# Kernel optimization log

Hardware: AMD Instinct MI355X
Metric: run time of the kernel (lower is better)

Reference implementation:

```python
import jax, jax.numpy as jnp
import numpy as np

HEADS = 8
POINTS = 4
EPS = 1e-5


def _layernorm(x, w, b):
    m = jnp.mean(x, axis=-1, keepdims=True)
    v = jnp.var(x, axis=-1, keepdims=True)
    return (x - m) / jnp.sqrt(v + EPS) * w + b


def _msdeform_attn(x, ref, value, H, W, Wv, bv, Woff, boff, Wa, ba, Wout, bout):
    # x: (N, Lq, C) queries; value: (N, H*W, C); ref: (N, Lq, 1, 2) in [0,1]
    N, Lq, C = x.shape
    hd = C // HEADS
    # value projection, split heads -> (N, heads, HW, hd)
    v = (value @ Wv + bv).reshape(N, H * W, HEADS, hd).transpose(0, 2, 1, 3)
    # per-query learned offsets and attention weights
    off = (x @ Woff + boff).reshape(N, Lq, HEADS, POINTS, 2)
    attw = jax.nn.softmax((x @ Wa + ba).reshape(N, Lq, HEADS, POINTS), axis=-1)
    offset_normalizer = jnp.array([W, H], dtype=x.dtype)
    # sampling locations in normalized [0,1] coords: (N, Lq, heads, points, 2)
    loc = ref[:, :, None, :, :] + off / offset_normalizer
    # grid_sample bilinear, align_corners=False, zeros padding: pixel = loc*size - 0.5
    gx = loc[..., 0] * W - 0.5
    gy = loc[..., 1] * H - 0.5
    x0 = jnp.floor(gx)
    y0 = jnp.floor(gy)
    wx = gx - x0
    wy = gy - y0
    x0i = x0.astype(jnp.int32)
    y0i = y0.astype(jnp.int32)

    def gather(xi, yi):  # (N,Lq,heads,points) int -> (N,heads,Lq,points,hd), zero outside
        valid = ((xi >= 0) & (xi < W) & (yi >= 0) & (yi < H))
        idx = (jnp.clip(yi, 0, H - 1) * W + jnp.clip(xi, 0, W - 1)).transpose(0, 2, 1, 3)
        g = jnp.take_along_axis(v, idx.reshape(N, HEADS, Lq * POINTS)[..., None], axis=2)
        return g.reshape(N, HEADS, Lq, POINTS, hd) * valid.transpose(0, 2, 1, 3)[..., None].astype(v.dtype)

    def cw(w_):  # corner weight to (N,heads,Lq,points,1)
        return w_.transpose(0, 2, 1, 3)[..., None]

    samp = (gather(x0i, y0i) * cw((1 - wx) * (1 - wy))
            + gather(x0i + 1, y0i) * cw(wx * (1 - wy))
            + gather(x0i, y0i + 1) * cw((1 - wx) * wy)
            + gather(x0i + 1, y0i + 1) * cw(wx * wy))
    out = jnp.einsum('nhlpd,nlhp->nlhd', samp, attw).reshape(N, Lq, C)
    return out @ Wout + bout


def setup_inputs() -> dict:
    key = jax.random.key(0)
    ks = jax.random.split(key, 12)
    N, Lq, C, H, W = 4, 6400, 256, 80, 80
    hid = 4 * C
    hp2 = HEADS * POINTS * 2
    hp = HEADS * POINTS

    def w(k, shape, s=0.02):
        return jax.random.normal(k, shape, dtype=jnp.float32) * s

    return {
        'x': jax.random.normal(ks[0], (N, Lq, C), dtype=jnp.float32),
        'ref': jax.random.uniform(ks[1], (N, Lq, 1, 2), dtype=jnp.float32),
        'value': jax.random.normal(ks[2], (N, Lq, C), dtype=jnp.float32),
        'H': H, 'W': W,
        'ln1_w': jnp.ones((C,), jnp.float32), 'ln1_b': jnp.zeros((C,), jnp.float32),
        'ln2_w': jnp.ones((C,), jnp.float32), 'ln2_b': jnp.zeros((C,), jnp.float32),
        'Wv': w(ks[3], (C, C)), 'bv': jnp.zeros((C,), jnp.float32),
        'Woff': w(ks[4], (C, hp2), 0.01), 'boff': w(ks[5], (hp2,), 0.5),
        'Wa': w(ks[6], (C, hp)), 'ba': jnp.zeros((hp,), jnp.float32),
        'Wout': w(ks[7], (C, C)), 'bout': jnp.zeros((C,), jnp.float32),
        'W1': w(ks[8], (C, hid)), 'b1': jnp.zeros((hid,), jnp.float32),
        'W2': w(ks[9], (hid, C)), 'b2': jnp.zeros((C,), jnp.float32),
    }


def reference(x, ref, value, H, W, ln1_w, ln1_b, ln2_w, ln2_b, Wv, bv, Woff, boff, Wa, ba, Wout, bout, W1, b1, W2, b2):
    # x = x + attn(norm1(x), ref, value); LayerScale/DropPath are identity (init_values=None, drop_path=0)
    a = _msdeform_attn(_layernorm(x, ln1_w, ln1_b), ref, value, H, W, Wv, bv, Woff, boff, Wa, ba, Wout, bout)
    x = x + a
    # x = x + mlp(norm2(x))
    h = _layernorm(x, ln2_w, ln2_b)
    h = jax.nn.gelu(h @ W1 + b1, approximate=False)
    return x + (h @ W2 + b2)
```

## Files before the change

### kernel.cpp

```cpp
#include <hip/hip_runtime.h>

#define NB    4
#define LQ    6400
#define CC    256
#define HH    80
#define WW    80
#define HWSZ  (HH*WW)
#define RTOT  (NB*LQ)
#define HID   1024

typedef __attribute__((ext_vector_type(8))) short bf16x8;
typedef __attribute__((ext_vector_type(4))) float f32x4;

__device__ __forceinline__ float bf2f(unsigned short u) {
    unsigned int i = ((unsigned int)u) << 16;
    float f; __builtin_memcpy(&f, &i, 4); return f;
}
__device__ __forceinline__ unsigned short f2bf(float f) {
    unsigned int i; __builtin_memcpy(&i, &f, 4);
    unsigned int r = i + 0x7fffu + ((i >> 16) & 1u);
    return (unsigned short)(r >> 16);
}

__global__ void cvt_k(const float* __restrict__ in, unsigned short* __restrict__ out, int n4) {
    int i = blockIdx.x * 256 + threadIdx.x;
    if (i < n4) {
        float4 u = ((const float4*)in)[i];
        ushort4 o;
        o.x = f2bf(u.x); o.y = f2bf(u.y); o.z = f2bf(u.z); o.w = f2bf(u.w);
        ((ushort4*)out)[i] = o;
    }
}

__global__ void transpose_cvt_k(const float* __restrict__ B,
                                unsigned short* __restrict__ Bt, int K, int N) {
    int idx = blockIdx.x * 256 + threadIdx.x;
    if (idx < K * N) {
        int n = idx / K;
        int k = idx - n * K;
        Bt[idx] = f2bf(B[k * N + n]);
    }
}

__global__ void swizzle_k(const float* __restrict__ src, unsigned short* __restrict__ dst,
                          int K, int N) {
    int g = blockIdx.x * 256 + threadIdx.x;
    if (g >= (K / 8) * N) return;
    int n  = g % N;
    int kq = g / N;
    int kbase = (kq >> 2) * 32 + (kq & 3) * 8;
    unsigned short* d = dst + (size_t)g * 8;
    #pragma unroll
    for (int j = 0; j < 8; ++j)
        d[j] = f2bf(src[(size_t)(kbase + j) * N + n]);
}

__global__ void bias_cat_k(const float* __restrict__ boff, const float* __restrict__ ba,
                           float* __restrict__ out) {
    int i = threadIdx.x;
    if (i < 64) out[i] = boff[i];
    else if (i < 96) out[i] = ba[i - 64];
}

__global__ void ln_k(const float* __restrict__ x,
                     const float* __restrict__ w,
                     const float* __restrict__ b,
                     unsigned short* __restrict__ y) {
    int row  = blockIdx.x * 4 + (threadIdx.x >> 6);
    int lane = threadIdx.x & 63;
    const float* xr = x + (size_t)row * CC + lane * 4;
    float4 u = *(const float4*)xr;
    float s  = u.x + u.y + u.z + u.w;
    float s2 = u.x*u.x + u.y*u.y + u.z*u.z + u.w*u.w;
    #pragma unroll
    for (int m = 1; m < 64; m <<= 1) {
        s  += __shfl_xor(s,  m);
        s2 += __shfl_xor(s2, m);
    }
    float mean = s * (1.0f / CC);
    float var  = s2 * (1.0f / CC) - mean * mean;
    float rstd = rsqrtf(fmaxf(var, 0.0f) + 1e-5f);
    float4 uw = *(const float4*)(w + lane * 4);
    float4 ub = *(const float4*)(b + lane * 4);
    ushort4 o;
    o.x = f2bf((u.x - mean) * rstd * uw.x + ub.x);
    o.y = f2bf((u.y - mean) * rstd * uw.y + ub.y);
    o.z = f2bf((u.z - mean) * rstd * uw.z + ub.z);
    o.w = f2bf((u.w - mean) * rstd * uw.w + ub.w);
    *(ushort4*)(y + (size_t)row * CC + lane * 4) = o;
}

template<int EPI, bool OF32>
__global__ __launch_bounds__(256) void gemm_t(const unsigned short* __restrict__ A,
                                              const unsigned short* __restrict__ Bt,
                                              const float* __restrict__ bias,
                                              const float* __restrict__ res,
                                              void* __restrict__ Cout_,
                                              int M, int Nv, int K) {
    __shared__ unsigned short Als[64 * 32];
    __shared__ unsigned short Bls[128 * 32];
    int lane = threadIdx.x & 63;
    int wave = threadIdx.x >> 6;
    int quad = lane >> 4;
    int l16  = lane & 15;
    int m0 = blockIdx.x * 64;
    int n0 = blockIdx.y * 128;
    int wm = (wave & 1) * 32;
    int wn = (wave >> 1) * 64;

    f32x4 acc[2][4];
    #pragma unroll
    for (int i = 0; i < 2; ++i)
        #pragma unroll
        for (int j = 0; j < 4; ++j)
            acc[i][j] = (f32x4){0.f, 0.f, 0.f, 0.f};

    int srow = lane >> 2;
    int scol = (lane & 3) * 8;
    const unsigned short* Ag = A  + (size_t)(m0 + wave * 16 + srow) * K + scol;
    const unsigned short* Bg = Bt + (size_t)(n0 + wave * 32 + srow) * K + scol;
    unsigned short* Alp = &Als[wave * 512];
    unsigned short* Blp = &Bls[wave * 1024];

    for (int k0 = 0; k0 < K; k0 += 32) {
        __syncthreads();
        __builtin_amdgcn_global_load_lds(
            (const __attribute__((address_space(1))) void*)(Ag + k0),
            (__attribute__((address_space(3))) void*)Alp, 16, 0, 0);
        #pragma unroll
        for (int t = 0; t < 2; ++t) {
            __builtin_amdgcn_global_load_lds(
                (const __attribute__((address_space(1))) void*)(Bg + (size_t)t * 16 * K + k0),
                (__attribute__((address_space(3))) void*)(Blp + t * 512), 16, 0, 0);
        }
        __builtin_amdgcn_s_waitcnt(0);
        __syncthreads();

        bf16x8 af[2], bfr[4];
        #pragma unroll
        for (int i = 0; i < 2; ++i)
            af[i] = *(const bf16x8*)&Als[(wm + i * 16 + l16) * 32 + quad * 8];
        #pragma unroll
        for (int j = 0; j < 4; ++j)
            bfr[j] = *(const bf16x8*)&Bls[(wn + j * 16 + l16) * 32 + quad * 8];
        #pragma unroll
        for (int i = 0; i < 2; ++i)
            #pragma unroll
            for (int j = 0; j < 4; ++j)
                acc[i][j] = __builtin_amdgcn_mfma_f32_16x16x32_bf16(af[i], bfr[j], acc[i][j], 0, 0, 0);
    }

    #pragma unroll
    for (int j = 0; j < 4; ++j) {
        int cbase = n0 + wn + j * 16;
        if (cbase >= Nv) continue;
        int col = cbase + l16;
        float bv = bias[col];
        #pragma unroll
        for (int i = 0; i < 2; ++i) {
            #pragma unroll
            for (int r = 0; r < 4; ++r) {
                int row = m0 + wm + i * 16 + quad * 4 + r;
                float val = acc[i][j][r] + bv;
                if (EPI == 2) val += res[(size_t)row * Nv + col];
                if (OF32) ((float*)Cout_)[(size_t)row * Nv + col] = val;
                else      ((unsigned short*)Cout_)[(size_t)row * Nv + col] = f2bf(val);
            }
        }
    }
}

__global__ __launch_bounds__(256) void sample_k(
        const unsigned short* __restrict__ v,
        const float* __restrict__ ref,
        const unsigned short* __restrict__ oa,
        unsigned short* __restrict__ samp) {
    __shared__ int4   sidx[256];
    __shared__ float4 sw[256];

    int t = threadIdx.x;
    int row0 = blockIdx.x * 8;
    int n = blockIdx.x / (LQ / 8);

    {
        int q = t >> 5;
        int h = (t >> 2) & 7;
        int p = t & 3;
        int row = row0 + q;
        float refx = ref[row * 2 + 0];
        float refy = ref[row * 2 + 1];
        const unsigned short* oar = oa + (size_t)row * 96;
        float ox = bf2f(oar[(h * 4 + p) * 2 + 0]);
        float oy = bf2f(oar[(h * 4 + p) * 2 + 1]);
        float l  = bf2f(oar[64 + h * 4 + p]);
        float m = fmaxf(l, __shfl_xor(l, 1));
        m = fmaxf(m, __shfl_xor(m, 2));
        float e = __expf(l - m);
        float s = e + __shfl_xor(e, 1);
        s = s + __shfl_xor(s, 2);
        float wp = e / s;

        float gx = (refx + ox * (1.0f / WW)) * WW - 0.5f;
        float gy = (refy + oy * (1.0f / HH)) * HH - 0.5f;
        float fx = floorf(gx), fy = floorf(gy);
        float wx = gx - fx, wy = gy - fy;
        int x0 = (int)fx, y0 = (int)fy;
        int x1 = x0 + 1, y1 = y0 + 1;
        bool vx0 = (unsigned)x0 < WW, vx1 = (unsigned)x1 < WW;
        bool vy0 = (unsigned)y0 < HH, vy1 = (unsigned)y1 < HH;
        float w00 = (vx0 && vy0) ? wp * (1.f - wx) * (1.f - wy) : 0.f;
        float w10 = (vx1 && vy0) ? wp * wx * (1.f - wy)         : 0.f;
        float w01 = (vx0 && vy1) ? wp * (1.f - wx) * wy         : 0.f;
        float w11 = (vx1 && vy1) ? wp * wx * wy                 : 0.f;
        int cx0 = min(max(x0, 0), WW - 1), cx1 = min(max(x1, 0), WW - 1);
        int cy0 = min(max(y0, 0), HH - 1), cy1 = min(max(y1, 0), HH - 1);
        sidx[t] = (int4){cy0 * WW + cx0, cy0 * WW + cx1, cy1 * WW + cx0, cy1 * WW + cx1};
        sw[t]   = (float4){w00, w10, w01, w11};
    }
    __syncthreads();

    int q  = t >> 5;
    int sub = t & 31;
    int h  = sub >> 2;
    int cg = sub & 3;
    int row = row0 + q;
    const unsigned short* base = v + (size_t)n * HWSZ * CC + h * 32 + cg * 8;

    float acc[8];
    #pragma unroll
    for (int j = 0; j < 8; ++j) acc[j] = 0.f;

    #pragma unroll
    for (int p = 0; p < 4; ++p) {
        int e = ((q * 8 + h) * 4) + p;
        int4   I = sidx[e];
        float4 Wt = sw[e];
        const int* Ip = (const int*)&I;
        const float* Wp = (const float*)&Wt;
        #pragma unroll
        for (int c = 0; c < 4; ++c) {
            bf16x8 u = *(const bf16x8*)(base + (size_t)Ip[c] * CC);
            float wgt = Wp[c];
            #pragma unroll
            for (int j = 0; j < 8; ++j)
                acc[j] += wgt * bf2f((unsigned short)u[j]);
        }
    }

    bf16x8 o;
    #pragma unroll
    for (int j = 0; j < 8; ++j) o[j] = (short)f2bf(acc[j]);
    *(bf16x8*)(samp + (size_t)row * CC + h * 32 + cg * 8) = o;
}

__global__ __launch_bounds__(512) void mlp_k(
        const float* __restrict__ x2,
        const float* __restrict__ lw,
        const float* __restrict__ lb,
        const unsigned short* __restrict__ w1s,
        const float* __restrict__ b1,
        const unsigned short* __restrict__ w2s,
        const float* __restrict__ b2,
        float* __restrict__ out) {
    __shared__ char lds_raw[66560];
    unsigned short* hblob = (unsigned short*)lds_raw;
    unsigned short* h1b0  = (unsigned short*)(lds_raw + 33280);
    unsigned short* h1b1  = (unsigned short*)(lds_raw + 49920);
    float* trans = (float*)lds_raw;

    int t = threadIdx.x;
    int lane = t & 63, wave = t >> 6;
    int quad = lane >> 4, l16 = lane & 15;
    int row0 = blockIdx.x * 64;

    {
        int r = t >> 3, sub = t & 7;
        const float* xr = x2 + (size_t)(row0 + r) * CC;
        float4 xv[4][2];
        float s = 0.f, s2 = 0.f;
        #pragma unroll
        for (int jj = 0; jj < 4; ++jj) {
            #pragma unroll
            for (int u = 0; u < 2; ++u) {
                float4 v = *(const float4*)(xr + sub * 8 + jj * 64 + u * 4);
                xv[jj][u] = v;
                s  += v.x + v.y + v.z + v.w;
                s2 += v.x*v.x + v.y*v.y + v.z*v.z + v.w*v.w;
            }
        }
        #pragma unroll
        for (int m = 1; m < 8; m <<= 1) {
            s  += __shfl_xor(s,  m);
            s2 += __shfl_xor(s2, m);
        }
        float mean = s * (1.0f / CC);
        float var  = s2 * (1.0f / CC) - mean * mean;
        float rstd = rsqrtf(fmaxf(var, 0.0f) + 1e-5f);
        #pragma unroll
        for (int jj = 0; jj < 4; ++jj) {
            int c0 = sub * 8 + jj * 64;
            float4 w0 = *(const float4*)(lw + c0);
            float4 w1 = *(const float4*)(lw + c0 + 4);
            float4 bb0 = *(const float4*)(lb + c0);
            float4 bb1 = *(const float4*)(lb + c0 + 4);
            bf16x8 o;
            o[0] = (short)f2bf((xv[jj][0].x - mean) * rstd * w0.x + bb0.x);
            o[1] = (short)f2bf((xv[jj][0].y - mean) * rstd * w0.y + bb0.y);
            o[2] = (short)f2bf((xv[jj][0].z - mean) * rstd * w0.z + bb0.z);
            o[3] = (short)f2bf((xv[jj][0].w - mean) * rstd * w0.w + bb0.w);
            o[4] = (short)f2bf((xv[jj][1].x - mean) * rstd * w1.x + bb1.x);
            o[5] = (short)f2bf((xv[jj][1].y - mean) * rstd * w1.y + bb1.y);
            o[6] = (short)f2bf((xv[jj][1].z - mean) * rstd * w1.z + bb1.z);
            o[7] = (short)f2bf((xv[jj][1].w - mean) * rstd * w1.w + bb1.w);
            int kq = sub + jj * 8;
            *(bf16x8*)((char*)hblob + kq * 1040 + r * 16) = o;
        }
    }
    __syncthreads();

    f32x4 acc2[2][4];
    #pragma unroll
    for (int a = 0; a < 2; ++a)
        #pragma unroll
        for (int b = 0; b < 4; ++b)
            acc2[a][b] = (f32x4){0.f, 0.f, 0.f, 0.f};

    auto s1 = [&](int hc, unsigned short* dst) {
        f32x4 a[4];
        #pragma unroll
        for (int qt = 0; qt < 4; ++qt) a[qt] = (f32x4){0.f, 0.f, 0.f, 0.f};
        #pragma unroll
        for (int kb = 0; kb < 8; ++kb) {
            bf16x8 a1 = *(const bf16x8*)(w1s + ((size_t)(kb * 4 + quad) * 1024 + hc * 128 + wave * 16 + l16) * 8);
            #pragma unroll
            for (int qt = 0; qt < 4; ++qt) {
                bf16x8 bf = *(const bf16x8*)((char*)hblob + (kb * 4 + quad) * 1040 + (qt * 16 + l16) * 16);
                a[qt] = __builtin_amdgcn_mfma_f32_16x16x32_bf16(a1, bf, a[qt], 0, 0, 0);
            }
        }
        int hl = wave * 16 + quad * 4;
        float4 bb = *(const float4*)(b1 + hc * 128 + hl);
        const float* bp = (const float*)&bb;
        #pragma unroll
        for (int qt = 0; qt < 4; ++qt) {
            unsigned long long pk = 0;
            #pragma unroll
            for (int r = 0; r < 4; ++r) {
                float val = a[qt][r] + bp[r];
                val = 0.5f * val * (1.0f + erff(val * 0.70710678118654752f));
                pk |= ((unsigned long long)f2bf(val)) << (16 * r);
            }
            *(unsigned long long*)((char*)dst + (hl >> 3) * 1040 + (qt * 16 + l16) * 16 + (hl & 7) * 2) = pk;
        }
    };

    auto s2 = [&](int hc, const unsigned short* src) {
        #pragma unroll
        for (int k2 = 0; k2 < 4; ++k2) {
            bf16x8 a2[2], bf[4];
            #pragma unroll
            for (int ct = 0; ct < 2; ++ct)
                a2[ct] = *(const bf16x8*)(w2s + ((size_t)((hc * 4 + k2) * 4 + quad) * 256 + wave * 32 + ct * 16 + l16) * 8);
            #pragma unroll
            for (int qt = 0; qt < 4; ++qt)
                bf[qt] = *(const bf16x8*)((const char*)src + (k2 * 4 + quad) * 1040 + (qt * 16 + l16) * 16);
            #pragma unroll
            for (int ct = 0; ct < 2; ++ct)
                #pragma unroll
                for (int qt = 0; qt < 4; ++qt)
                    acc2[ct][qt] = __builtin_amdgcn_mfma_f32_16x16x32_bf16(a2[ct], bf[qt], acc2[ct][qt], 0, 0, 0);
        }
    };

    s1(0, h1b0);
    for (int hc = 0; hc < 8; ++hc) {
        __syncthreads();
        const unsigned short* cur = (hc & 1) ? h1b1 : h1b0;
        unsigned short*       nxt = (hc & 1) ? h1b0 : h1b1;
        s2(hc, cur);
        if (hc < 7) s1(hc + 1, nxt);
    }
    __syncthreads();

    #pragma unroll
    for (int qt = 0; qt < 4; ++qt) {
        int qrow = qt * 16 + l16;
        #pragma unroll
        for (int ct = 0; ct < 2; ++ct) {
            int c4 = wave * 8 + ct * 4 + quad;
            *(f32x4*)(trans + qrow * 260 + c4 * 4) = acc2[ct][qt];
        }
    }
    __syncthreads();
    {
        int rr = t >> 3;
        int c4b = t & 7;
        int row = row0 + rr;
        #pragma unroll
        for (int i = 0; i < 8; ++i) {
            int c4 = i * 8 + c4b;
            f32x4 v = *(const f32x4*)(trans + rr * 260 + c4 * 4);
            int c = c4 * 4;
            float4 xv = *(const float4*)(x2 + (size_t)row * CC + c);
            float4 bb = *(const float4*)(b2 + c);
            float4 o;
            o.x = v[0] + xv.x + bb.x;
            o.y = v[1] + xv.y + bb.y;
            o.z = v[2] + xv.z + bb.z;
            o.w = v[3] + xv.w + bb.w;
            *(float4*)(out + (size_t)row * CC + c) = o;
        }
    }
}

extern "C" void kernel_launch(void* const* d_in, const int* in_sizes, int n_in,
                              void* d_out, int out_size, void* d_ws, size_t ws_size,
                              hipStream_t stream) {
    const float* x     = (const float*)d_in[0];
    const float* ref   = (const float*)d_in[1];
    const float* value = (const float*)d_in[2];
    const float* ln1w  = (const float*)d_in[5];
    const float* ln1b  = (const float*)d_in[6];
    const float* ln2w  = (const float*)d_in[7];
    const float* ln2b  = (const float*)d_in[8];
    const float* Wv    = (const float*)d_in[9];
    const float* bv    = (const float*)d_in[10];
    const float* Woff  = (const float*)d_in[11];
    const float* boff  = (const float*)d_in[12];
    const float* Wa    = (const float*)d_in[13];
    const float* ba    = (const float*)d_in[14];
    const float* Wout  = (const float*)d_in[15];
    const float* bout  = (const float*)d_in[16];
    const float* W1    = (const float*)d_in[17];
    const float* b1    = (const float*)d_in[18];
    const float* W2    = (const float*)d_in[19];
    const float* b2    = (const float*)d_in[20];

    char* ws = (char*)d_ws;
    unsigned short* wt_v  = (unsigned short*)(ws + 0);
    unsigned short* wt_o  = (unsigned short*)(ws + 131072);
    unsigned short* w1s_b = (unsigned short*)(ws + 262144);
    unsigned short* w2s_b = (unsigned short*)(ws + 786432);
    unsigned short* wt_oa = (unsigned short*)(ws + 1310720);
    float*          b_oa  = (float*)         (ws + 1376256);
    float*          x2_f  = (float*)         (ws + 1376768);
    unsigned short* val_b = (unsigned short*)(ws + 40698368);
    unsigned short* smp_b = (unsigned short*)(ws + 40698368);
    unsigned short* xn_b  = (unsigned short*)(ws + 53805568);
    unsigned short* v_b   = (unsigned short*)(ws + 66912768);
    unsigned short* oa_b  = (unsigned short*)(ws + 80019968);

    transpose_cvt_k<<<(256*256 + 255) / 256, 256, 0, stream>>>(Wv,   wt_v,           256, 256);
    transpose_cvt_k<<<(256*256 + 255) / 256, 256, 0, stream>>>(Wout, wt_o,           256, 256);
    transpose_cvt_k<<<(256*64  + 255) / 256, 256, 0, stream>>>(Woff, wt_oa,          256, 64);
    transpose_cvt_k<<<(256*32  + 255) / 256, 256, 0, stream>>>(Wa,   wt_oa + 64*256, 256, 32);
    swizzle_k<<<128, 256, 0, stream>>>(W1, w1s_b, 256, 1024);
    swizzle_k<<<128, 256, 0, stream>>>(W2, w2s_b, 1024, 256);
    bias_cat_k<<<1, 128, 0, stream>>>(boff, ba, b_oa);

    cvt_k<<<(RTOT*CC/4 + 255) / 256, 256, 0, stream>>>(value, val_b, RTOT*CC/4);
    ln_k<<<RTOT / 4, 256, 0, stream>>>(x, ln1w, ln1b, xn_b);

    dim3 blk(256);
    gemm_t<0, false><<<dim3(RTOT/64, 2), blk, 0, stream>>>(val_b, wt_v,  bv,   nullptr, v_b,  RTOT, 256,  256);
    gemm_t<0, false><<<dim3(RTOT/64, 1), blk, 0, stream>>>(xn_b,  wt_oa, b_oa, nullptr, oa_b, RTOT, 96,   256);
    sample_k<<<RTOT / 8, 256, 0, stream>>>(v_b, ref, oa_b, smp_b);
    gemm_t<2, true ><<<dim3(RTOT/64, 2), blk, 0, stream>>>(smp_b, wt_o,  bout, x,       x2_f, RTOT, 256,  256);
    mlp_k<<<RTOT / 64, 512, 0, stream>>>(x2_f, ln2w, ln2b, w1s_b, b1, w2s_b, b2, (float*)d_out);
}
```

Before: 248.3 us.

## Fuse LN1 with offset/attn GEMM and sampling with output projection

Merges the seven weight-prep launches into a single prep kernel. It fuses LayerNorm1 with the offset/attention-logit projection into one MFMA kernel, and fuses bilinear sampling with the Wout projection and residual add. The sampled tile stays in LDS, so neither the normalized activations nor the sampled features make a round trip through global memory. Sample indices are packed to short4 to save LDS. The cost is larger LDS per block, fewer resident blocks, and idle waves in the 96-column GEMM.

```diff
diff --git a/kernel.cpp b/kernel.cpp
--- a/kernel.cpp
+++ b/kernel.cpp
@@ -32,62 +32,109 @@
     }
 }
 
-__global__ void transpose_cvt_k(const float* __restrict__ B,
-                                unsigned short* __restrict__ Bt, int K, int N) {
+__global__ void prep_k(const float* __restrict__ Wv,   const float* __restrict__ Wout,
+                       const float* __restrict__ W1,   const float* __restrict__ W2,
+                       const float* __restrict__ Woff, const float* __restrict__ Wa,
+                       const float* __restrict__ boff, const float* __restrict__ ba,
+                       unsigned short* __restrict__ wtv,  unsigned short* __restrict__ woutS,
+                       unsigned short* __restrict__ w1s,  unsigned short* __restrict__ w2s,
+                       unsigned short* __restrict__ woas, float* __restrict__ b_oa) {
     int idx = blockIdx.x * 256 + threadIdx.x;
-    if (idx < K * N) {
-        int n = idx / K;
-        int k = idx - n * K;
-        Bt[idx] = f2bf(B[k * N + n]);
-    }
-}
-
-__global__ void swizzle_k(const float* __restrict__ src, unsigned short* __restrict__ dst,
-                          int K, int N) {
-    int g = blockIdx.x * 256 + threadIdx.x;
-    if (g >= (K / 8) * N) return;
-    int n  = g % N;
-    int kq = g / N;
-    int kbase = (kq >> 2) * 32 + (kq & 3) * 8;
-    unsigned short* d = dst + (size_t)g * 8;
-    #pragma unroll
-    for (int j = 0; j < 8; ++j)
-        d[j] = f2bf(src[(size_t)(kbase + j) * N + n]);
-}
-
-__global__ void bias_cat_k(const float* __restrict__ boff, const float* __restrict__ ba,
-                           float* __restrict__ out) {
-    int i = threadIdx.x;
-    if (i < 64) out[i] = boff[i];
-    else if (i < 96) out[i] = ba[i - 64];
-}
-
-__global__ void ln_k(const float* __restrict__ x,
-                     const float* __restrict__ w,
-                     const float* __restrict__ b,
-                     unsigned short* __restrict__ y) {
-    int row  = blockIdx.x * 4 + (threadIdx.x >> 6);
-    int lane = threadIdx.x & 63;
-    const float* xr = x + (size_t)row * CC + lane * 4;
-    float4 u = *(const float4*)xr;
-    float s  = u.x + u.y + u.z + u.w;
-    float s2 = u.x*u.x + u.y*u.y + u.z*u.z + u.w*u.w;
-    #pragma unroll
-    for (int m = 1; m < 64; m <<= 1) {
+    if (idx < 65536) {
+        int n = idx >> 8, k = idx & 255;
+        wtv[idx] = f2bf(Wv[(size_t)k * 256 + n]);
+        return;
+    }
+    idx -= 65536;
+    if (idx < 32768) {
+        int n = idx & 1023, kq = idx >> 10;
+        int kb = (kq >> 2) * 32 + (kq & 3) * 8;
+        unsigned short* d = w1s + (size_t)idx * 8;
+        #pragma unroll
+        for (int j = 0; j < 8; ++j) d[j] = f2bf(W1[(size_t)(kb + j) * 1024 + n]);
+        return;
+    }
+    idx -= 32768;
+    if (idx < 32768) {
+        int n = idx & 255, kq = idx >> 8;
+        int kb = (kq >> 2) * 32 + (kq & 3) * 8;
+        unsigned short* d = w2s + (size_t)idx * 8;
+        #pragma unroll
+        for (int j = 0; j < 8; ++j) d[j] = f2bf(W2[(size_t)(kb + j) * 256 + n]);
+        return;
+    }
+    idx -= 32768;
+    if (idx < 8192) {
+        int n = idx & 255, kq = idx >> 8;
+        int kb = (kq >> 2) * 32 + (kq & 3) * 8;
+        unsigned short* d = woutS + (size_t)idx * 8;
+        #pragma unroll
+        for (int j = 0; j < 8; ++j) d[j] = f2bf(Wout[(size_t)(kb + j) * 256 + n]);
+        return;
+    }
+    idx -= 8192;
+    if (idx < 4096) {
+        int n = idx & 127, kq = idx >> 7;
+        int kb = (kq >> 2) * 32 + (kq & 3) * 8;
+        unsigned short* d = woas + (size_t)idx * 8;
+        #pragma unroll
+        for (int j = 0; j < 8; ++j) {
+            float v = 0.f;
+            if (n < 64)      v = Woff[(size_t)(kb + j) * 64 + n];
+            else if (n < 96) v = Wa[(size_t)(kb + j) * 32 + (n - 64)];
+            d[j] = f2bf(v);
+        }
+        return;
+    }
+    idx -= 4096;
+    if (idx < 96) b_oa[idx] = idx < 64 ? boff[idx] : ba[idx - 64];
+}
+
+__device__ __forceinline__ void ln_stage(const float* __restrict__ xbase,
+                                         const float* __restrict__ lw,
+                                         const float* __restrict__ lb,
+                                         unsigned short* hblob, int t) {
+    int r = t >> 3, sub = t & 7;
+    const float* xr = xbase + (size_t)r * CC;
+    float4 xv[4][2];
+    float s = 0.f, s2 = 0.f;
+    #pragma unroll
+    for (int jj = 0; jj < 4; ++jj) {
+        #pragma unroll
+        for (int u = 0; u < 2; ++u) {
+            float4 v = *(const float4*)(xr + sub * 8 + jj * 64 + u * 4);
+            xv[jj][u] = v;
+            s  += v.x + v.y + v.z + v.w;
+            s2 += v.x*v.x + v.y*v.y + v.z*v.z + v.w*v.w;
+        }
+    }
+    #pragma unroll
+    for (int m = 1; m < 8; m <<= 1) {
         s  += __shfl_xor(s,  m);
         s2 += __shfl_xor(s2, m);
     }
     float mean = s * (1.0f / CC);
     float var  = s2 * (1.0f / CC) - mean * mean;
     float rstd = rsqrtf(fmaxf(var, 0.0f) + 1e-5f);
-    float4 uw = *(const float4*)(w + lane * 4);
-    float4 ub = *(const float4*)(b + lane * 4);
-    ushort4 o;
-    o.x = f2bf((u.x - mean) * rstd * uw.x + ub.x);
-    o.y = f2bf((u.y - mean) * rstd * uw.y + ub.y);
-    o.z = f2bf((u.z - mean) * rstd * uw.z + ub.z);
-    o.w = f2bf((u.w - mean) * rstd * uw.w + ub.w);
-    *(ushort4*)(y + (size_t)row * CC + lane * 4) = o;
+    #pragma unroll
+    for (int jj = 0; jj < 4; ++jj) {
+        int c0 = sub * 8 + jj * 64;
+        float4 w0 = *(const float4*)(lw + c0);
+        float4 w1 = *(const float4*)(lw + c0 + 4);
+        float4 bb0 = *(const float4*)(lb + c0);
+        float4 bb1 = *(const float4*)(lb + c0 + 4);
+        bf16x8 o;
+        o[0] = (short)f2bf((xv[jj][0].x - mean) * rstd * w0.x + bb0.x);
+        o[1] = (short)f2bf((xv[jj][0].y - mean) * rstd * w0.y + bb0.y);
+        o[2] = (short)f2bf((xv[jj][0].z - mean) * rstd * w0.z + bb0.z);
+        o[3] = (short)f2bf((xv[jj][0].w - mean) * rstd * w0.w + bb0.w);
+        o[4] = (short)f2bf((xv[jj][1].x - mean) * rstd * w1.x + bb1.x);
+        o[5] = (short)f2bf((xv[jj][1].y - mean) * rstd * w1.y + bb1.y);
+        o[6] = (short)f2bf((xv[jj][1].z - mean) * rstd * w1.z + bb1.z);
+        o[7] = (short)f2bf((xv[jj][1].w - mean) * rstd * w1.w + bb1.w);
+        int kq = sub + jj * 8;
+        *(bf16x8*)((char*)hblob + kq * 1040 + r * 16) = o;
+    }
 }
 
 template<int EPI, bool OF32>
@@ -170,87 +217,191 @@
     }
 }
 
-__global__ __launch_bounds__(256) void sample_k(
+__global__ __launch_bounds__(512) void lnoa_k(
+        const float* __restrict__ x, const float* __restrict__ lw, const float* __restrict__ lb,
+        const unsigned short* __restrict__ woas, const float* __restrict__ b_oa,
+        unsigned short* __restrict__ oa) {
+    __shared__ char lds_raw[33280];
+    unsigned short* hblob = (unsigned short*)lds_raw;
+    int t = threadIdx.x;
+    int lane = t & 63, wave = t >> 6;
+    int quad = lane >> 4, l16 = lane & 15;
+    int row0 = blockIdx.x * 64;
+
+    ln_stage(x + (size_t)row0 * CC, lw, lb, hblob, t);
+    __syncthreads();
+
+    if (wave < 6) {
+        f32x4 acc[4];
+        #pragma unroll
+        for (int qt = 0; qt < 4; ++qt) acc[qt] = (f32x4){0.f, 0.f, 0.f, 0.f};
+        #pragma unroll
+        for (int kb = 0; kb < 8; ++kb) {
+            bf16x8 a1 = *(const bf16x8*)(woas + ((size_t)(kb * 4 + quad) * 128 + wave * 16 + l16) * 8);
+            #pragma unroll
+            for (int qt = 0; qt < 4; ++qt) {
+                bf16x8 bf = *(const bf16x8*)((char*)hblob + (kb * 4 + quad) * 1040 + (qt * 16 + l16) * 16);
+                acc[qt] = __builtin_amdgcn_mfma_f32_16x16x32_bf16(a1, bf, acc[qt], 0, 0, 0);
+            }
+        }
+        int n0 = wave * 16 + quad * 4;
+        float4 bb = *(const float4*)(b_oa + n0);
+        const float* bp = (const float*)&bb;
+        #pragma unroll
+        for (int qt = 0; qt < 4; ++qt) {
+            unsigned long long pk = 0;
+            #pragma unroll
+            for (int r = 0; r < 4; ++r)
+                pk |= ((unsigned long long)f2bf(acc[qt][r] + bp[r])) << (16 * r);
+            *(unsigned long long*)(oa + (size_t)(row0 + qt * 16 + l16) * 96 + n0) = pk;
+        }
+    }
+}
+
+__global__ __launch_bounds__(512) void samwout_k(
         const unsigned short* __restrict__ v,
         const float* __restrict__ ref,
         const unsigned short* __restrict__ oa,
-        unsigned short* __restrict__ samp) {
-    __shared__ int4   sidx[256];
-    __shared__ float4 sw[256];
+        const unsigned short* __restrict__ woutS,
+        const float* __restrict__ bout,
+        const float* __restrict__ x,
+        float* __restrict__ x2) {
+    __shared__ char lds_raw[57856];
+    unsigned short* hblob = (unsigned short*)lds_raw;
+    short4* sidx = (short4*)(lds_raw + 33280);
+    float4* sw   = (float4*)(lds_raw + 41472);
+    float* trans = (float*)lds_raw;
 
     int t = threadIdx.x;
-    int row0 = blockIdx.x * 8;
-    int n = blockIdx.x / (LQ / 8);
-
-    {
-        int q = t >> 5;
-        int h = (t >> 2) & 7;
-        int p = t & 3;
-        int row = row0 + q;
-        float refx = ref[row * 2 + 0];
-        float refy = ref[row * 2 + 1];
-        const unsigned short* oar = oa + (size_t)row * 96;
-        float ox = bf2f(oar[(h * 4 + p) * 2 + 0]);
-        float oy = bf2f(oar[(h * 4 + p) * 2 + 1]);
-        float l  = bf2f(oar[64 + h * 4 + p]);
-        float m = fmaxf(l, __shfl_xor(l, 1));
-        m = fmaxf(m, __shfl_xor(m, 2));
-        float e = __expf(l - m);
-        float s = e + __shfl_xor(e, 1);
-        s = s + __shfl_xor(s, 2);
-        float wp = e / s;
-
-        float gx = (refx + ox * (1.0f / WW)) * WW - 0.5f;
-        float gy = (refy + oy * (1.0f / HH)) * HH - 0.5f;
-        float fx = floorf(gx), fy = floorf(gy);
-        float wx = gx - fx, wy = gy - fy;
-        int x0 = (int)fx, y0 = (int)fy;
-        int x1 = x0 + 1, y1 = y0 + 1;
-        bool vx0 = (unsigned)x0 < WW, vx1 = (unsigned)x1 < WW;
-        bool vy0 = (unsigned)y0 < HH, vy1 = (unsigned)y1 < HH;
-        float w00 = (vx0 && vy0) ? wp * (1.f - wx) * (1.f - wy) : 0.f;
-        float w10 = (vx1 && vy0) ? wp * wx * (1.f - wy)         : 0.f;
-        float w01 = (vx0 && vy1) ? wp * (1.f - wx) * wy         : 0.f;
-        float w11 = (vx1 && vy1) ? wp * wx * wy                 : 0.f;
-        int cx0 = min(max(x0, 0), WW - 1), cx1 = min(max(x1, 0), WW - 1);
-        int cy0 = min(max(y0, 0), HH - 1), cy1 = min(max(y1, 0), HH - 1);
-        sidx[t] = (int4){cy0 * WW + cx0, cy0 * WW + cx1, cy1 * WW + cx0, cy1 * WW + cx1};
-        sw[t]   = (float4){w00, w10, w01, w11};
-    }
-    __syncthreads();
-
-    int q  = t >> 5;
-    int sub = t & 31;
-    int h  = sub >> 2;
-    int cg = sub & 3;
-    int row = row0 + q;
-    const unsigned short* base = v + (size_t)n * HWSZ * CC + h * 32 + cg * 8;
-
-    float acc[8];
-    #pragma unroll
-    for (int j = 0; j < 8; ++j) acc[j] = 0.f;
-
-    #pragma unroll
-    for (int p = 0; p < 4; ++p) {
-        int e = ((q * 8 + h) * 4) + p;
-        int4   I = sidx[e];
-        float4 Wt = sw[e];
-        const int* Ip = (const int*)&I;
-        const float* Wp = (const float*)&Wt;
-        #pragma unroll
-        for (int c = 0; c < 4; ++c) {
-            bf16x8 u = *(const bf16x8*)(base + (size_t)Ip[c] * CC);
-            float wgt = Wp[c];
-            #pragma unroll
-            for (int j = 0; j < 8; ++j)
-                acc[j] += wgt * bf2f((unsigned short)u[j]);
-        }
-    }
-
-    bf16x8 o;
-    #pragma unroll
-    for (int j = 0; j < 8; ++j) o[j] = (short)f2bf(acc[j]);
-    *(bf16x8*)(samp + (size_t)row * CC + h * 32 + cg * 8) = o;
+    int lane = t & 63, wave = t >> 6;
+    int quad = lane >> 4, l16 = lane & 15;
+    int row0 = blockIdx.x * 64;
+    int nb = blockIdx.x / (LQ / 64);
+
+    for (int half = 0; half < 2; ++half) {
+        int rbase = half * 32;
+        #pragma unroll
+        for (int s = 0; s < 2; ++s) {
+            int e = t + s * 512;
+            int q = e >> 5, sub = e & 31, h = sub >> 2, p = sub & 3;
+            int row = row0 + rbase + q;
+            float refx = ref[row * 2 + 0];
+            float refy = ref[row * 2 + 1];
+            const unsigned short* oar = oa + (size_t)row * 96;
+            float ox = bf2f(oar[(h * 4 + p) * 2 + 0]);
+            float oy = bf2f(oar[(h * 4 + p) * 2 + 1]);
+            float l  = bf2f(oar[64 + h * 4 + p]);
+            float m = fmaxf(l, __shfl_xor(l, 1));
+            m = fmaxf(m, __shfl_xor(m, 2));
+            float ee = __expf(l - m);
+            float ss = ee + __shfl_xor(ee, 1);
+            ss = ss + __shfl_xor(ss, 2);
+            float wp = ee / ss;
+
+            float gx = (refx + ox * (1.0f / WW)) * WW - 0.5f;
+            float gy = (refy + oy * (1.0f / HH)) * HH - 0.5f;
+            float fx = floorf(gx), fy = floorf(gy);
+            float wx = gx - fx, wy = gy - fy;
+            int x0 = (int)fx, y0 = (int)fy;
+            int x1 = x0 + 1, y1 = y0 + 1;
+            bool vx0 = (unsigned)x0 < WW, vx1 = (unsigned)x1 < WW;
+            bool vy0 = (unsigned)y0 < HH, vy1 = (unsigned)y1 < HH;
+            float w00 = (vx0 && vy0) ? wp * (1.f - wx) * (1.f - wy) : 0.f;
+            float w10 = (vx1 && vy0) ? wp * wx * (1.f - wy)         : 0.f;
+            float w01 = (vx0 && vy1) ? wp * (1.f - wx) * wy         : 0.f;
+            float w11 = (vx1 && vy1) ? wp * wx * wy                 : 0.f;
+            int cx0 = min(max(x0, 0), WW - 1), cx1 = min(max(x1, 0), WW - 1);
+            int cy0 = min(max(y0, 0), HH - 1), cy1 = min(max(y1, 0), HH - 1);
+            sidx[e] = (short4){(short)(cy0 * WW + cx0), (short)(cy0 * WW + cx1),
+                               (short)(cy1 * WW + cx0), (short)(cy1 * WW + cx1)};
+            sw[e]   = (float4){w00, w10, w01, w11};
+        }
+        __syncthreads();
+        #pragma unroll
+        for (int s = 0; s < 2; ++s) {
+            int c = t + s * 512;
+            int q = c >> 5, sub = c & 31, h = sub >> 2, cg = sub & 3;
+            const unsigned short* base = v + (size_t)nb * HWSZ * CC + h * 32 + cg * 8;
+            float acc[8];
+            #pragma unroll
+            for (int j = 0; j < 8; ++j) acc[j] = 0.f;
+            #pragma unroll
+            for (int p = 0; p < 4; ++p) {
+                int e = q * 32 + h * 4 + p;
+                short4 I = sidx[e];
+                float4 Wt = sw[e];
+                const short* Ip = (const short*)&I;
+                const float* Wp = (const float*)&Wt;
+                #pragma unroll
+                for (int cn = 0; cn < 4; ++cn) {
+                    bf16x8 u = *(const bf16x8*)(base + (size_t)(unsigned short)Ip[cn] * CC);
+                    float wgt = Wp[cn];
+                    #pragma unroll
+                    for (int j = 0; j < 8; ++j)
+                        acc[j] += wgt * bf2f((unsigned short)u[j]);
+                }
+            }
+            bf16x8 o;
+            #pragma unroll
+            for (int j = 0; j < 8; ++j) o[j] = (short)f2bf(acc[j]);
+            *(bf16x8*)((char*)hblob + sub * 1040 + (rbase + q) * 16) = o;
+        }
+        __syncthreads();
+    }
+
+    f32x4 acc2[2][4];
+    #pragma unroll
+    for (int a = 0; a < 2; ++a)
+        #pragma unroll
+        for (int b = 0; b < 4; ++b)
+            acc2[a][b] = (f32x4){0.f, 0.f, 0.f, 0.f};
+    #pragma unroll
+    for (int kb = 0; kb < 8; ++kb) {
+        bf16x8 a2[2], bf[4];
+        #pragma unroll
+        for (int ct = 0; ct < 2; ++ct)
+            a2[ct] = *(const bf16x8*)(woutS + ((size_t)(kb * 4 + quad) * 256 + wave * 32 + ct * 16 + l16) * 8);
+        #pragma unroll
+        for (int qt = 0; qt < 4; ++qt)
+            bf[qt] = *(const bf16x8*)((char*)hblob + (kb * 4 + quad) * 1040 + (qt * 16 + l16) * 16);
+        #pragma unroll
+        for (int ct = 0; ct < 2; ++ct)
+            #pragma unroll
+            for (int qt = 0; qt < 4; ++qt)
+                acc2[ct][qt] = __builtin_amdgcn_mfma_f32_16x16x32_bf16(a2[ct], bf[qt], acc2[ct][qt], 0, 0, 0);
+    }
+
+    for (int p = 0; p < 2; ++p) {
+        __syncthreads();
+        #pragma unroll
+        for (int qi = 0; qi < 2; ++qi) {
+            int qt = p * 2 + qi;
+            int qlocal = qt * 16 + l16 - p * 32;
+            #pragma unroll
+            for (int ct = 0; ct < 2; ++ct) {
+                int c4 = wave * 8 + ct * 4 + quad;
+                *(f32x4*)(trans + qlocal * 260 + c4 * 4) = acc2[ct][qt];
+            }
+        }
+        __syncthreads();
+        int rr = t >> 4;
+        int c4b = t & 15;
+        int row = row0 + p * 32 + rr;
+        #pragma unroll
+        for (int i = 0; i < 4; ++i) {
+            int c4 = i * 16 + c4b;
+            f32x4 vv = *(const f32x4*)(trans + rr * 260 + c4 * 4);
+            int c = c4 * 4;
+            float4 xv = *(const float4*)(x + (size_t)row * CC + c);
+            float4 bb = *(const float4*)(bout + c);
+            float4 o;
+            o.x = vv[0] + xv.x + bb.x;
+            o.y = vv[1] + xv.y + bb.y;
+            o.z = vv[2] + xv.z + bb.z;
+            o.w = vv[3] + xv.w + bb.w;
+            *(float4*)(x2 + (size_t)row * CC + c) = o;
+        }
+    }
 }
 
 __global__ __launch_bounds__(512) void mlp_k(
@@ -273,49 +424,7 @@
     int quad = lane >> 4, l16 = lane & 15;
     int row0 = blockIdx.x * 64;
 
-    {
-        int r = t >> 3, sub = t & 7;
-        const float* xr = x2 + (size_t)(row0 + r) * CC;
-        float4 xv[4][2];
-        float s = 0.f, s2 = 0.f;
-        #pragma unroll
-        for (int jj = 0; jj < 4; ++jj) {
-            #pragma unroll
-            for (int u = 0; u < 2; ++u) {
-                float4 v = *(const float4*)(xr + sub * 8 + jj * 64 + u * 4);
-                xv[jj][u] = v;
-                s  += v.x + v.y + v.z + v.w;
-                s2 += v.x*v.x + v.y*v.y + v.z*v.z + v.w*v.w;
-            }
-        }
-        #pragma unroll
-        for (int m = 1; m < 8; m <<= 1) {
-            s  += __shfl_xor(s,  m);
-            s2 += __shfl_xor(s2, m);
-        }
-        float mean = s * (1.0f / CC);
-        float var  = s2 * (1.0f / CC) - mean * mean;
-        float rstd = rsqrtf(fmaxf(var, 0.0f) + 1e-5f);
-        #pragma unroll
-        for (int jj = 0; jj < 4; ++jj) {
-            int c0 = sub * 8 + jj * 64;
-            float4 w0 = *(const float4*)(lw + c0);
-            float4 w1 = *(const float4*)(lw + c0 + 4);
-            float4 bb0 = *(const float4*)(lb + c0);
-            float4 bb1 = *(const float4*)(lb + c0 + 4);
-            bf16x8 o;
-            o[0] = (short)f2bf((xv[jj][0].x - mean) * rstd * w0.x + bb0.x);
-            o[1] = (short)f2bf((xv[jj][0].y - mean) * rstd * w0.y + bb0.y);
-            o[2] = (short)f2bf((xv[jj][0].z - mean) * rstd * w0.z + bb0.z);
-            o[3] = (short)f2bf((xv[jj][0].w - mean) * rstd * w0.w + bb0.w);
-            o[4] = (short)f2bf((xv[jj][1].x - mean) * rstd * w1.x + bb1.x);
-            o[5] = (short)f2bf((xv[jj][1].y - mean) * rstd * w1.y + bb1.y);
-            o[6] = (short)f2bf((xv[jj][1].z - mean) * rstd * w1.z + bb1.z);
-            o[7] = (short)f2bf((xv[jj][1].w - mean) * rstd * w1.w + bb1.w);
-            int kq = sub + jj * 8;
-            *(bf16x8*)((char*)hblob + kq * 1040 + r * 16) = o;
-        }
-    }
+    ln_stage(x2 + (size_t)row0 * CC, lw, lb, hblob, t);
     __syncthreads();
 
     f32x4 acc2[2][4];
@@ -437,34 +546,22 @@
     const float* b2    = (const float*)d_in[20];
 
     char* ws = (char*)d_ws;
-    unsigned short* wt_v  = (unsigned short*)(ws + 0);
-    unsigned short* wt_o  = (unsigned short*)(ws + 131072);
-    unsigned short* w1s_b = (unsigned short*)(ws + 262144);
-    unsigned short* w2s_b = (unsigned short*)(ws + 786432);
-    unsigned short* wt_oa = (unsigned short*)(ws + 1310720);
-    float*          b_oa  = (float*)         (ws + 1376256);
-    float*          x2_f  = (float*)         (ws + 1376768);
-    unsigned short* val_b = (unsigned short*)(ws + 40698368);
-    unsigned short* smp_b = (unsigned short*)(ws + 40698368);
-    unsigned short* xn_b  = (unsigned short*)(ws + 53805568);
-    unsigned short* v_b   = (unsigned short*)(ws + 66912768);
-    unsigned short* oa_b  = (unsigned short*)(ws + 80019968);
-
-    transpose_cvt_k<<<(256*256 + 255) / 256, 256, 0, stream>>>(Wv,   wt_v,           256, 256);
-    transpose_cvt_k<<<(256*256 + 255) / 256, 256, 0, stream>>>(Wout, wt_o,           256, 256);
-    transpose_cvt_k<<<(256*64  + 255) / 256, 256, 0, stream>>>(Woff, wt_oa,          256, 64);
-    transpose_cvt_k<<<(256*32  + 255) / 256, 256, 0, stream>>>(Wa,   wt_oa + 64*256, 256, 32);
-    swizzle_k<<<128, 256, 0, stream>>>(W1, w1s_b, 256, 1024);
-    swizzle_k<<<128, 256, 0, stream>>>(W2, w2s_b, 1024, 256);
-    bias_cat_k<<<1, 128, 0, stream>>>(boff, ba, b_oa);
-
+    unsigned short* wtv_b  = (unsigned short*)(ws + 0);
+    unsigned short* wouts_b= (unsigned short*)(ws + 131072);
+    unsigned short* w1s_b  = (unsigned short*)(ws + 262144);
+    unsigned short* w2s_b  = (unsigned short*)(ws + 786432);
+    unsigned short* woas_b = (unsigned short*)(ws + 1310720);
+    float*          b_oa   = (float*)         (ws + 1376256);
+    float*          x2_f   = (float*)         (ws + 1376768);
+    unsigned short* val_b  = (unsigned short*)(ws + 27591168);
+    unsigned short* v_b    = (unsigned short*)(ws + 40698368);
+    unsigned short* oa_b   = (unsigned short*)(ws + 53805568);
+
+    prep_k<<<561, 256, 0, stream>>>(Wv, Wout, W1, W2, Woff, Wa, boff, ba,
+                                    wtv_b, wouts_b, w1s_b, w2s_b, woas_b, b_oa);
     cvt_k<<<(RTOT*CC/4 + 255) / 256, 256, 0, stream>>>(value, val_b, RTOT*CC/4);
-    ln_k<<<RTOT / 4, 256, 0, stream>>>(x, ln1w, ln1b, xn_b);
-
-    dim3 blk(256);
-    gemm_t<0, false><<<dim3(RTOT/64, 2), blk, 0, stream>>>(val_b, wt_v,  bv,   nullptr, v_b,  RTOT, 256,  256);
-    gemm_t<0, false><<<dim3(RTOT/64, 1), blk, 0, stream>>>(xn_b,  wt_oa, b_oa, nullptr, oa_b, RTOT, 96,   256);
-    sample_k<<<RTOT / 8, 256, 0, stream>>>(v_b, ref, oa_b, smp_b);
-    gemm_t<2, true ><<<dim3(RTOT/64, 2), blk, 0, stream>>>(smp_b, wt_o,  bout, x,       x2_f, RTOT, 256,  256);
-    mlp_k<<<RTOT / 64, 512, 0, stream>>>(x2_f, ln2w, ln2b, w1s_b, b1, w2s_b, b2, (float*)d_out);
-}
+    gemm_t<0, false><<<dim3(RTOT/64, 2), 256, 0, stream>>>(val_b, wtv_b, bv, nullptr, v_b, RTOT, 256, 256);
+    lnoa_k<<<RTOT/64, 512, 0, stream>>>(x, ln1w, ln1b, woas_b, b_oa, oa_b);
+    samwout_k<<<RTOT/64, 512, 0, stream>>>(v_b, ref, oa_b, wouts_b, bout, x, x2_f);
+    mlp_k<<<RTOT/64, 512, 0, stream>>>(x2_f, ln2w, ln2b, w1s_b, b1, w2s_b, b2, (float*)d_out);
+}
```

After: 224.6 us. 1.11x faster.
